# Performance work log

Measured on AMD Instinct MI355X. Metric: run time of the kernel, lower is better.

The kernel has to match this reference:

```python
import jax, jax.numpy as jnp
import numpy as np

BATCH = 32      # init batch_size
HID = 256       # init hidden_dim
SENT = 64       # sentence_size
WORDS = 64      # words per sentence (the -1 in the view)
N = BATCH * SENT


def setup_inputs() -> dict:
    key = jax.random.key(0)
    k1, k2, k3, k4 = jax.random.split(key, 4)
    stdv_lin = 1.0 / np.sqrt(HID)
    x = jax.random.normal(k1, (N, WORDS, HID), dtype=jnp.float32)
    W = jax.random.uniform(k2, (HID, HID), jnp.float32, -stdv_lin, stdv_lin)
    b = jax.random.uniform(k3, (HID,), jnp.float32, -stdv_lin, stdv_lin)
    context = jax.random.uniform(k4, (HID,), jnp.float32, -stdv_lin, stdv_lin)
    return {"x": x, "W": W, "b": b, "context": context, "sentence_size": SENT}


def reference(x, W, b, context, sentence_size):
    # tanh(Linear(x)) applied per position; vectorized over the batch loop
    attends = jnp.tanh(jnp.einsum("nwh,oh->nwo", x, W) + b)  # [N, WORDS, HID]
    scores = attends * context                                 # [N, WORDS, HID]
    # nn.Softmax on the [-1, HID] view -> softmax over the hidden dim
    alpha = jax.nn.softmax(scores, axis=-1)                    # [N, WORDS, HID]
    attended = x * alpha                                       # legacy same-numel mul
    attended = attended.reshape(BATCH, sentence_size, -1, HID)
    return jnp.sum(attended, axis=2)                           # [BATCH, SENT, HID]
```

## Files before the change

kernel.cpp:

```cpp
#include <hip/hip_runtime.h>
#include <hip/hip_bf16.h>

#define HID 256
#define NROWS 2048
#define NITER 8
#define GRID (NROWS / NITER)
#define PITCH 264
#define AS1 __attribute__((address_space(1)))
#define AS3 __attribute__((address_space(3)))

typedef __attribute__((ext_vector_type(8))) short short8;
typedef __attribute__((ext_vector_type(4))) float float4v;
typedef __attribute__((ext_vector_type(4))) unsigned short ushort4v;

__device__ __forceinline__ float bf2f(unsigned short u) {
    return __uint_as_float(((unsigned int)u) << 16);
}

__device__ __forceinline__ unsigned int pk_bf16(float a, float b) {
    __hip_bfloat162 p = __float22bfloat162_rn(float2{a, b});
    return *(unsigned int*)&p;
}

__device__ __forceinline__ float tanh_fast(float x) {
    float e = __builtin_amdgcn_exp2f(x * 2.8853900817779268f);
    return 1.0f - 2.0f * __builtin_amdgcn_rcpf(e + 1.0f);
}

__device__ __forceinline__ float exp_small(float s) {
    float p = __builtin_fmaf(s, 0.16666667f, 0.5f);
    p = __builtin_fmaf(p, s, 1.0f);
    return __builtin_fmaf(p, s, 1.0f);
}

__device__ __forceinline__ float row16_sum(float v) {
    float t;
    t = __builtin_bit_cast(float, __builtin_amdgcn_update_dpp(
            0, __builtin_bit_cast(int, v), 0xB1, 0xf, 0xf, true));
    v += t;
    t = __builtin_bit_cast(float, __builtin_amdgcn_update_dpp(
            0, __builtin_bit_cast(int, v), 0x4E, 0xf, 0xf, true));
    v += t;
    t = __builtin_bit_cast(float, __builtin_amdgcn_update_dpp(
            0, __builtin_bit_cast(int, v), 0x124, 0xf, 0xf, true));
    v += t;
    t = __builtin_bit_cast(float, __builtin_amdgcn_update_dpp(
            0, __builtin_bit_cast(int, v), 0x128, 0xf, 0xf, true));
    v += t;
    return v;
}

__global__ void cvt_w(const float* __restrict__ W, unsigned short* __restrict__ Wb) {
    int i = blockIdx.x * 256 + threadIdx.x;
    float4v v = ((const float4v*)W)[i];
    unsigned int lo = pk_bf16(v.x, v.y), hi = pk_bf16(v.z, v.w);
    ushort4v u;
    u.x = (unsigned short)lo; u.y = (unsigned short)(lo >> 16);
    u.z = (unsigned short)hi; u.w = (unsigned short)(hi >> 16);
    ((ushort4v*)Wb)[i] = u;
}

__global__ __launch_bounds__(512, 2) void attend_fused(
    const float* __restrict__ x, const unsigned short* __restrict__ Wb,
    const float* __restrict__ bias, const float* __restrict__ ctx,
    float* __restrict__ out)
{
    __shared__ float fstage[64 * 256];
    __shared__ unsigned short xs[64 * PITCH];
    __shared__ float wsum[8][64];
    __shared__ float rinv[64];

    const int tid  = threadIdx.x;
    const int wave = tid >> 6;
    const int lane = tid & 63;
    const int q    = lane >> 4;
    const int c    = lane & 15;
    const int obase = wave * 32;

    float bb[2], cc[2];
#pragma unroll
    for (int nt = 0; nt < 2; ++nt) {
        bb[nt] = bias[obase + 2 * c + nt];
        cc[nt] = ctx[obase + 2 * c + nt];
    }
    short8 bfrag[8][2];
#pragma unroll
    for (int nt = 0; nt < 2; ++nt) {
        const unsigned short* wr = &Wb[(size_t)(obase + 2 * c + nt) * 256 + q * 8];
#pragma unroll
        for (int kt = 0; kt < 8; ++kt)
            bfrag[kt][nt] = *(const short8*)(wr + kt * 32);
    }

    const int n0 = blockIdx.x * NITER;

    {
        const float* xn = x + (size_t)n0 * (64 * 256);
#pragma unroll
        for (int t = 0; t < 8; ++t) {
            const int row = wave * 8 + t;
            __builtin_amdgcn_global_load_lds((const AS1 void*)(xn + row * 256 + lane * 4),
                                             (AS3 void*)&fstage[row * 256], 16, 0, 0);
        }
    }

    for (int it = 0; it < NITER; ++it) {
        const int n = n0 + it;
        const float* xnext = x + (size_t)(n + 1) * (64 * 256);
        const bool pf = (it + 1 < NITER);

        __syncthreads();

#pragma unroll
        for (int i = 0; i < 8; ++i) {
            const int chunk = tid + 512 * i;
            const int r = chunk >> 6, col4 = (chunk & 63) * 4;
            float4v v = *(const float4v*)&fstage[chunk * 4];
            uint2 u;
            u.x = pk_bf16(v.x, v.y);
            u.y = pk_bf16(v.z, v.w);
            *(uint2*)&xs[r * PITCH + col4] = u;
        }
        __syncthreads();

        if (pf) {
#pragma unroll
            for (int t = 0; t < 4; ++t) {
                const int row = wave * 8 + t;
                __builtin_amdgcn_global_load_lds((const AS1 void*)(xnext + row * 256 + lane * 4),
                                                 (AS3 void*)&fstage[row * 256], 16, 0, 0);
            }
        }

        float4v acc[4][2];
#pragma unroll
        for (int mt = 0; mt < 4; ++mt)
#pragma unroll
            for (int nt = 0; nt < 2; ++nt)
                acc[mt][nt] = (float4v){0.f, 0.f, 0.f, 0.f};

#pragma unroll
        for (int kt = 0; kt < 8; ++kt) {
            short8 a[4];
#pragma unroll
            for (int mt = 0; mt < 4; ++mt)
                a[mt] = *(const short8*)&xs[(mt * 16 + c) * PITCH + kt * 32 + q * 8];
#pragma unroll
            for (int nt = 0; nt < 2; ++nt)
#pragma unroll
                for (int mt = 0; mt < 4; ++mt)
                    acc[mt][nt] = __builtin_amdgcn_mfma_f32_16x16x32_bf16(
                        a[mt], bfrag[kt][nt], acc[mt][nt], 0, 0, 0);
        }

        float psum[4][4];
#pragma unroll
        for (int mt = 0; mt < 4; ++mt)
#pragma unroll
            for (int r = 0; r < 4; ++r)
                psum[mt][r] = 0.f;

#pragma unroll
        for (int nt = 0; nt < 2; ++nt) {
#pragma unroll
            for (int mt = 0; mt < 4; ++mt) {
#pragma unroll
                for (int r = 0; r < 4; ++r) {
                    float s = tanh_fast(acc[mt][nt][r] + bb[nt]) * cc[nt];
                    float e = exp_small(s);
                    acc[mt][nt][r] = e;
                    psum[mt][r] += e;
                }
            }
        }
#pragma unroll
        for (int mt = 0; mt < 4; ++mt)
#pragma unroll
            for (int r = 0; r < 4; ++r)
                psum[mt][r] = row16_sum(psum[mt][r]);
        if (c == 0) {
#pragma unroll
            for (int mt = 0; mt < 4; ++mt)
#pragma unroll
                for (int r = 0; r < 4; ++r)
                    wsum[wave][mt * 16 + q * 4 + r] = psum[mt][r];
        }
        __syncthreads();
        if (tid < 64) {
            float t = wsum[0][tid] + wsum[1][tid] + wsum[2][tid] + wsum[3][tid]
                    + wsum[4][tid] + wsum[5][tid] + wsum[6][tid] + wsum[7][tid];
            rinv[tid] = __builtin_amdgcn_rcpf(t);
        }
        __syncthreads();

        if (pf) {
#pragma unroll
            for (int t = 4; t < 8; ++t) {
                const int row = wave * 8 + t;
                __builtin_amdgcn_global_load_lds((const AS1 void*)(xnext + row * 256 + lane * 4),
                                                 (AS3 void*)&fstage[row * 256], 16, 0, 0);
            }
        }

        float ri[4][4];
#pragma unroll
        for (int mt = 0; mt < 4; ++mt)
#pragma unroll
            for (int r = 0; r < 4; ++r)
                ri[mt][r] = rinv[mt * 16 + q * 4 + r];

        float outp[2] = {0.f, 0.f};
#pragma unroll
        for (int mt = 0; mt < 4; ++mt) {
#pragma unroll
            for (int r = 0; r < 4; ++r) {
                const int w = mt * 16 + q * 4 + r;
                unsigned int pair = *(const unsigned int*)&xs[w * PITCH + obase + 2 * c];
                const float wgt = ri[mt][r];
                outp[0] += bf2f((unsigned short)pair)         * (acc[mt][0][r] * wgt);
                outp[1] += bf2f((unsigned short)(pair >> 16)) * (acc[mt][1][r] * wgt);
            }
        }
#pragma unroll
        for (int nt = 0; nt < 2; ++nt) {
            float v = outp[nt];
            v += __shfl_xor(v, 16);
            v += __shfl_xor(v, 32);
            outp[nt] = v;
        }
        if (q == 0)
            *(float2*)&out[(size_t)n * HID + obase + 2 * c] = float2{outp[0], outp[1]};
    }
}

extern "C" void kernel_launch(void* const* d_in, const int* in_sizes, int n_in,
                              void* d_out, int out_size, void* d_ws, size_t ws_size,
                              hipStream_t stream) {
    const float* x    = (const float*)d_in[0];
    const float* W    = (const float*)d_in[1];
    const float* bias = (const float*)d_in[2];
    const float* ctx  = (const float*)d_in[3];
    unsigned short* Wb = (unsigned short*)d_ws;

    cvt_w<<<64, 256, 0, stream>>>(W, Wb);
    attend_fused<<<GRID, 512, 0, stream>>>(x, Wb, bias, ctx, (float*)d_out);
}
```

Baseline: 205.8 us.

## Prefetch next x tile into registers and double-buffer bf16 LDS tile

Replaces the fp32 LDS staging buffer filled by global_load_lds with register prefetch of the next x tile, converted to bf16 into a second LDS buffer at the end of each iteration. The mid-iteration barriers now wait only on LDS counters (lgkmcnt), so the outstanding global loads are not drained at each barrier. This removes one barrier per iteration and the fp32 staging round trip through LDS. In exchange it holds 32 extra VGPRs of prefetched data, which may pressure the 2-blocks-per-CU launch bound.

```diff
diff --git a/kernel.cpp b/kernel.cpp
--- a/kernel.cpp
+++ b/kernel.cpp
@@ -6,8 +6,6 @@
 #define NITER 8
 #define GRID (NROWS / NITER)
 #define PITCH 264
-#define AS1 __attribute__((address_space(1)))
-#define AS3 __attribute__((address_space(3)))
 
 typedef __attribute__((ext_vector_type(8))) short short8;
 typedef __attribute__((ext_vector_type(4))) float float4v;
@@ -31,6 +29,13 @@
     float p = __builtin_fmaf(s, 0.16666667f, 0.5f);
     p = __builtin_fmaf(p, s, 1.0f);
     return __builtin_fmaf(p, s, 1.0f);
+}
+
+__device__ __forceinline__ void barrier_lds_only() {
+    __asm__ volatile("" ::: "memory");
+    __builtin_amdgcn_s_waitcnt(0xC07F);
+    __builtin_amdgcn_s_barrier();
+    __asm__ volatile("" ::: "memory");
 }
 
 __device__ __forceinline__ float row16_sum(float v) {
@@ -65,8 +70,7 @@
     const float* __restrict__ bias, const float* __restrict__ ctx,
     float* __restrict__ out)
 {
-    __shared__ float fstage[64 * 256];
-    __shared__ unsigned short xs[64 * PITCH];
+    __shared__ unsigned short xs[2][64 * PITCH];
     __shared__ float wsum[8][64];
     __shared__ float rinv[64];
 
@@ -95,41 +99,33 @@
     const int n0 = blockIdx.x * NITER;
 
     {
-        const float* xn = x + (size_t)n0 * (64 * 256);
-#pragma unroll
-        for (int t = 0; t < 8; ++t) {
-            const int row = wave * 8 + t;
-            __builtin_amdgcn_global_load_lds((const AS1 void*)(xn + row * 256 + lane * 4),
-                                             (AS3 void*)&fstage[row * 256], 16, 0, 0);
-        }
-    }
-
-    for (int it = 0; it < NITER; ++it) {
-        const int n = n0 + it;
-        const float* xnext = x + (size_t)(n + 1) * (64 * 256);
-        const bool pf = (it + 1 < NITER);
-
-        __syncthreads();
-
+        const float4v* xg = (const float4v*)(x + (size_t)n0 * (64 * 256));
+        float4v v0[8];
+#pragma unroll
+        for (int i = 0; i < 8; ++i)
+            v0[i] = xg[tid + 512 * i];
 #pragma unroll
         for (int i = 0; i < 8; ++i) {
             const int chunk = tid + 512 * i;
             const int r = chunk >> 6, col4 = (chunk & 63) * 4;
-            float4v v = *(const float4v*)&fstage[chunk * 4];
             uint2 u;
-            u.x = pk_bf16(v.x, v.y);
-            u.y = pk_bf16(v.z, v.w);
-            *(uint2*)&xs[r * PITCH + col4] = u;
-        }
-        __syncthreads();
-
-        if (pf) {
-#pragma unroll
-            for (int t = 0; t < 4; ++t) {
-                const int row = wave * 8 + t;
-                __builtin_amdgcn_global_load_lds((const AS1 void*)(xnext + row * 256 + lane * 4),
-                                                 (AS3 void*)&fstage[row * 256], 16, 0, 0);
-            }
+            u.x = pk_bf16(v0[i].x, v0[i].y);
+            u.y = pk_bf16(v0[i].z, v0[i].w);
+            *(uint2*)&xs[0][r * PITCH + col4] = u;
+        }
+    }
+    __syncthreads();
+
+    for (int it = 0; it < NITER; ++it) {
+        const int n = n0 + it;
+        const int cur = it & 1;
+
+        float4v vbuf[8];
+        if (it + 1 < NITER) {
+            const float4v* xg = (const float4v*)(x + (size_t)(n + 1) * (64 * 256));
+#pragma unroll
+            for (int i = 0; i < 8; ++i)
+                vbuf[i] = xg[tid + 512 * i];
         }
 
         float4v acc[4][2];
@@ -144,7 +140,7 @@
             short8 a[4];
 #pragma unroll
             for (int mt = 0; mt < 4; ++mt)
-                a[mt] = *(const short8*)&xs[(mt * 16 + c) * PITCH + kt * 32 + q * 8];
+                a[mt] = *(const short8*)&xs[cur][(mt * 16 + c) * PITCH + kt * 32 + q * 8];
 #pragma unroll
             for (int nt = 0; nt < 2; ++nt)
 #pragma unroll
@@ -185,22 +181,13 @@
                 for (int r = 0; r < 4; ++r)
                     wsum[wave][mt * 16 + q * 4 + r] = psum[mt][r];
         }
-        __syncthreads();
+        barrier_lds_only();
         if (tid < 64) {
             float t = wsum[0][tid] + wsum[1][tid] + wsum[2][tid] + wsum[3][tid]
                     + wsum[4][tid] + wsum[5][tid] + wsum[6][tid] + wsum[7][tid];
             rinv[tid] = __builtin_amdgcn_rcpf(t);
         }
-        __syncthreads();
-
-        if (pf) {
-#pragma unroll
-            for (int t = 4; t < 8; ++t) {
-                const int row = wave * 8 + t;
-                __builtin_amdgcn_global_load_lds((const AS1 void*)(xnext + row * 256 + lane * 4),
-                                                 (AS3 void*)&fstage[row * 256], 16, 0, 0);
-            }
-        }
+        barrier_lds_only();
 
         float ri[4][4];
 #pragma unroll
@@ -215,7 +202,7 @@
 #pragma unroll
             for (int r = 0; r < 4; ++r) {
                 const int w = mt * 16 + q * 4 + r;
-                unsigned int pair = *(const unsigned int*)&xs[w * PITCH + obase + 2 * c];
+                unsigned int pair = *(const unsigned int*)&xs[cur][w * PITCH + obase + 2 * c];
                 const float wgt = ri[mt][r];
                 outp[0] += bf2f((unsigned short)pair)         * (acc[mt][0][r] * wgt);
                 outp[1] += bf2f((unsigned short)(pair >> 16)) * (acc[mt][1][r] * wgt);
@@ -230,6 +217,19 @@
         }
         if (q == 0)
             *(float2*)&out[(size_t)n * HID + obase + 2 * c] = float2{outp[0], outp[1]};
+
+        if (it + 1 < NITER) {
+#pragma unroll
+            for (int i = 0; i < 8; ++i) {
+                const int chunk = tid + 512 * i;
+                const int r = chunk >> 6, col4 = (chunk & 63) * 4;
+                uint2 u;
+                u.x = pk_bf16(vbuf[i].x, vbuf[i].y);
+                u.y = pk_bf16(vbuf[i].z, vbuf[i].w);
+                *(uint2*)&xs[cur ^ 1][r * PITCH + col4] = u;
+            }
+            __syncthreads();
+        }
     }
 }
 
```

Result: no change. 207.7 us (+0.9%).
